# Kernel tuning notes

Measured on AMD Instinct MI355X. Metric: run time of the kernel, lower is better.

The kernel has to match this reference:

```python
import jax, jax.numpy as jnp
import numpy as np

B, T, P, N, E = 8, 12, 1000, 20000, 60000
FP, FN, H = 32, 32, 12  # patch feats, node feats, horizon
IN_DIM = (FP + FN) * T
HID = IN_DIM


def setup_inputs() -> dict:
    key = jax.random.key(0)
    ks = jax.random.split(key, 8)
    patch_x = jax.random.normal(ks[0], (B, T, P, FP), dtype=jnp.float32)
    nodes_x = jax.random.normal(ks[1], (B, T, N, FN), dtype=jnp.float32)
    subgraphs_batch = jax.random.randint(ks[2], (E,), 0, P)
    subgraphs_nodes_mapper = jax.random.randint(ks[3], (E,), 0, N)
    # 2-layer MLP: Linear(IN_DIM->HID) + ReLU + Linear(HID->H), no final activation
    s1 = 1.0 / np.sqrt(IN_DIM)
    s2 = 1.0 / np.sqrt(HID)
    W1 = jax.random.uniform(ks[4], (IN_DIM, HID), minval=-s1, maxval=s1, dtype=jnp.float32)
    b1 = jax.random.uniform(ks[5], (HID,), minval=-s1, maxval=s1, dtype=jnp.float32)
    W2 = jax.random.uniform(ks[6], (HID, H), minval=-s2, maxval=s2, dtype=jnp.float32)
    b2 = jax.random.uniform(ks[7], (H,), minval=-s2, maxval=s2, dtype=jnp.float32)
    return {"patch_x": patch_x, "nodes_x": nodes_x,
            "subgraphs_batch": subgraphs_batch,
            "subgraphs_nodes_mapper": subgraphs_nodes_mapper,
            "W1": W1, "b1": b1, "W2": W2, "b2": b2}


def reference(patch_x, nodes_x, subgraphs_batch, subgraphs_nodes_mapper, W1, b1, W2, b2):
    # gather patch features per membership entry: (B,T,E,FP)
    gathered = patch_x[:, :, subgraphs_batch, :]
    # scatter-mean over entries into nodes (segment reduction on entry axis)
    g = jnp.transpose(gathered, (2, 0, 1, 3))  # (E,B,T,FP)
    sums = jax.ops.segment_sum(g, subgraphs_nodes_mapper, num_segments=N)  # (N,B,T,FP)
    counts = jax.ops.segment_sum(jnp.ones((E,), jnp.float32), subgraphs_nodes_mapper, num_segments=N)
    mean = sums / jnp.maximum(counts, 1.0)[:, None, None, None]
    patch_x_nodes = jnp.transpose(mean, (1, 2, 0, 3))  # (B,T,N,FP)
    # rearrange 'B t n f -> B n (t f)'
    pxn = jnp.transpose(patch_x_nodes, (0, 2, 1, 3)).reshape(B, N, T * FP)
    nx = jnp.transpose(nodes_x, (0, 2, 1, 3)).reshape(B, N, T * FN)
    mlp_in = jnp.concatenate([nx, pxn], axis=-1)  # (B,N,IN_DIM)
    h = jax.nn.relu(jnp.einsum('bnd,dh->bnh', mlp_in, W1) + b1)
    out = jnp.einsum('bnh,ho->bno', h, W2) + b2  # (B,N,H)
    return out
```

## Files before the change

kernel.cpp:

```cpp
#include <hip/hip_runtime.h>

#define B_ 8
#define T_ 12
#define P_ 1000
#define N_ 20000
#define E_ 60000
#define FP_ 32
#define FN_ 32
#define HO_ 12
#define IND 768
#define M_ (B_*N_)

typedef __attribute__((ext_vector_type(8))) short bf16x8;
typedef __attribute__((ext_vector_type(4))) float f32x4;

__device__ __forceinline__ unsigned short f2bf(float x) {
    union { float f; unsigned int u; } v; v.f = x;
    unsigned int u = v.u;
    u += 0x7fffu + ((u >> 16) & 1u);
    return (unsigned short)(u >> 16);
}

#define GLDS16(gp, lp) \
    __builtin_amdgcn_global_load_lds((const __attribute__((address_space(1))) void*)(gp), \
                                     (__attribute__((address_space(3))) void*)(lp), 16, 0, 0)

__global__ void k_count(const int* __restrict__ mapper, int* __restrict__ counts) {
    int e = blockIdx.x * 256 + threadIdx.x;
    if (e < E_) atomicAdd(&counts[mapper[e]], 1);
}

__global__ __launch_bounds__(1024) void k_scan(const int* __restrict__ counts,
                                               int* __restrict__ offsets,
                                               int* __restrict__ cursor) {
    __shared__ int ps[1024];
    const int tid = threadIdx.x;
    const int CH = 20;
    const int base = tid * CH;
    int s = 0;
    for (int i = 0; i < CH; ++i) { int idx = base + i; if (idx < N_) s += counts[idx]; }
    ps[tid] = s;
    __syncthreads();
    for (int off = 1; off < 1024; off <<= 1) {
        int v = ps[tid];
        int a = (tid >= off) ? ps[tid - off] : 0;
        __syncthreads();
        ps[tid] = v + a;
        __syncthreads();
    }
    int run = (tid > 0) ? ps[tid - 1] : 0;
    for (int i = 0; i < CH; ++i) {
        int idx = base + i;
        if (idx < N_) { offsets[idx] = run; cursor[idx] = run; run += counts[idx]; }
    }
    if (tid == 1023) offsets[N_] = ps[1023];
}

__global__ void k_scatter(const int* __restrict__ mapper, const int* __restrict__ batch,
                          int* __restrict__ cursor, int* __restrict__ edge_p) {
    int e = blockIdx.x * 256 + threadIdx.x;
    if (e < E_) {
        int pos = atomicAdd(&cursor[mapper[e]], 1);
        edge_p[pos] = batch[e];
    }
}

__global__ void k_wprep(const float* __restrict__ W1, const float* __restrict__ W2,
                        unsigned short* __restrict__ W1t, unsigned short* __restrict__ W2t) {
    int i = blockIdx.x * 256 + threadIdx.x;
    if (i < IND * IND) {
        int h = i / IND, d = i - h * IND;
        W1t[i] = f2bf(W1[d * IND + h]);
    } else {
        int j = i - IND * IND;
        if (j < 16 * IND) {
            int o = j / IND, k = j - o * IND;
            W2t[j] = (o < HO_) ? f2bf(W2[k * HO_ + o]) : (unsigned short)0;
        }
    }
}

__global__ __launch_bounds__(256) void k_stage(const float* __restrict__ patch_x,
                                               const float* __restrict__ nodes_x,
                                               const int* __restrict__ offsets,
                                               const int* __restrict__ edge_p,
                                               unsigned short* __restrict__ X) {
    const int gw = (blockIdx.x * 256 + threadIdx.x) >> 6;
    const int lane = threadIdx.x & 63;
    const int b = gw / N_;
    const int n = gw - b * N_;
    unsigned short* xr = X + (size_t)gw * IND;

    int tt[3], ff[3];
    #pragma unroll
    for (int j = 0; j < 3; ++j) {
        const int c = 2 * (j * 64 + lane);
        tt[j] = c >> 5; ff[j] = c & 31;
    }

    const float* nb = nodes_x + ((size_t)b * T_ * N_ + n) * FN_;
    #pragma unroll
    for (int j = 0; j < 3; ++j) {
        float2 v = *(const float2*)(nb + (size_t)tt[j] * (N_ * FN_) + ff[j]);
        unsigned int pk = (unsigned int)f2bf(v.x) | ((unsigned int)f2bf(v.y) << 16);
        *(unsigned int*)(xr + 2 * (j * 64 + lane)) = pk;
    }

    const int s = offsets[n];
    const int cnt = offsets[n + 1] - s;
    int p_l = 0;
    if (lane < cnt) p_l = edge_p[s + lane];
    float2 acc[3] = {{0.f,0.f},{0.f,0.f},{0.f,0.f}};
    const float* pb0 = patch_x + (size_t)b * (T_ * P_ * FP_);
    const int m = cnt < 64 ? cnt : 64;
    for (int q = 0; q < m; ++q) {
        const int p = __shfl(p_l, q);
        const float* pe = pb0 + p * FP_;
        #pragma unroll
        for (int j = 0; j < 3; ++j) {
            float2 v = *(const float2*)(pe + (size_t)tt[j] * (P_ * FP_) + ff[j]);
            acc[j].x += v.x; acc[j].y += v.y;
        }
    }
    for (int q = 64; q < cnt; ++q) {
        const int p = edge_p[s + q];
        const float* pe = pb0 + p * FP_;
        #pragma unroll
        for (int j = 0; j < 3; ++j) {
            float2 v = *(const float2*)(pe + (size_t)tt[j] * (P_ * FP_) + ff[j]);
            acc[j].x += v.x; acc[j].y += v.y;
        }
    }
    const float inv = cnt > 0 ? 1.0f / (float)cnt : 0.0f;
    #pragma unroll
    for (int j = 0; j < 3; ++j) {
        unsigned int pk = (unsigned int)f2bf(acc[j].x * inv) |
                          ((unsigned int)f2bf(acc[j].y * inv) << 16);
        *(unsigned int*)(xr + 384 + 2 * (j * 64 + lane)) = pk;
    }
}

__global__ __launch_bounds__(256, 2) void k_gemm1(const unsigned short* __restrict__ X,
                                                  const unsigned short* __restrict__ W1t,
                                                  const float* __restrict__ b1,
                                                  const unsigned short* __restrict__ W2t,
                                                  float* __restrict__ part) {
    __shared__ __align__(16) unsigned short smem[16384];
    unsigned short* As = smem;
    unsigned short* Bs = smem + 8192;
    unsigned short* Hs = smem;

    const int id = blockIdx.x;
    const int q8 = 7500 >> 3, r8 = 7500 & 7;
    const int xcd = id & 7, pos = id >> 3;
    const int nid = (xcd < r8) ? xcd * (q8 + 1) + pos
                               : r8 * (q8 + 1) + (xcd - r8) * q8 + pos;
    const int colt = nid % 6;
    const int rowt = nid / 6;
    const int col0 = colt * 128;
    const int row0 = rowt * 128;

    const int t = threadIdx.x;
    const int lane = t & 63;
    const int w = t >> 6;
    const int wr = w >> 1, wc = w & 1;
    const int l15 = lane & 15;
    const int lhi = lane >> 4;

    f32x4 acc[4][4] = {};

    for (int kt = 0; kt < 12; ++kt) {
        const int k0 = kt * 64;
        #pragma unroll
        for (int i = 0; i < 4; ++i) {
            const int f = i * 2048 + t * 8;
            GLDS16(X + (row0 + (f >> 6)) * IND + k0 + (f & 63), &As[f]);
        }
        #pragma unroll
        for (int i = 0; i < 4; ++i) {
            const int f = i * 2048 + t * 8;
            GLDS16(W1t + (col0 + (f >> 6)) * IND + k0 + (f & 63), &Bs[f]);
        }
        __syncthreads();
        #pragma unroll
        for (int kk = 0; kk < 2; ++kk) {
            const int ko = kk * 32 + lhi * 8;
            bf16x8 af[4], bfr[4];
            #pragma unroll
            for (int m = 0; m < 4; ++m)
                af[m] = *(const bf16x8*)&As[(wr * 64 + m * 16 + l15) * 64 + ko];
            #pragma unroll
            for (int n = 0; n < 4; ++n)
                bfr[n] = *(const bf16x8*)&Bs[(wc * 64 + n * 16 + l15) * 64 + ko];
            #pragma unroll
            for (int m = 0; m < 4; ++m)
                #pragma unroll
                for (int n = 0; n < 4; ++n)
                    acc[m][n] = __builtin_amdgcn_mfma_f32_16x16x32_bf16(af[m], bfr[n], acc[m][n], 0, 0, 0);
        }
        __syncthreads();
    }

    #pragma unroll
    for (int n = 0; n < 4; ++n) {
        const int lcol = wc * 64 + n * 16 + l15;
        const float bb = b1[col0 + lcol];
        #pragma unroll
        for (int m = 0; m < 4; ++m) {
            #pragma unroll
            for (int r = 0; r < 4; ++r) {
                const int lrow = wr * 64 + m * 16 + lhi * 4 + r;
                float v = acc[m][n][r] + bb;
                v = v > 0.f ? v : 0.f;
                Hs[lrow * 128 + lcol] = f2bf(v);
            }
        }
    }
    __syncthreads();

    f32x4 p0 = {}, p1 = {};
    #pragma unroll
    for (int kk = 0; kk < 4; ++kk) {
        const int ko = kk * 32 + lhi * 8;
        bf16x8 bw = *(const bf16x8*)&W2t[l15 * IND + col0 + ko];
        bf16x8 a0 = *(const bf16x8*)&Hs[(w * 32 + l15) * 128 + ko];
        bf16x8 a1 = *(const bf16x8*)&Hs[(w * 32 + 16 + l15) * 128 + ko];
        p0 = __builtin_amdgcn_mfma_f32_16x16x32_bf16(a0, bw, p0, 0, 0, 0);
        p1 = __builtin_amdgcn_mfma_f32_16x16x32_bf16(a1, bw, p1, 0, 0, 0);
    }
    if (l15 < HO_) {
        float* pp = part + (size_t)colt * ((size_t)M_ * HO_);
        #pragma unroll
        for (int r = 0; r < 4; ++r) {
            const int g0 = row0 + w * 32 + lhi * 4 + r;
            pp[(size_t)g0 * HO_ + l15] = p0[r];
            pp[(size_t)(g0 + 16) * HO_ + l15] = p1[r];
        }
    }
}

__global__ void k_reduce(const float* __restrict__ part, const float* __restrict__ b2,
                         float* __restrict__ out) {
    int i = blockIdx.x * 256 + threadIdx.x;
    if (i < M_ * HO_) {
        const int o = i % HO_;
        float s = b2[o];
        #pragma unroll
        for (int ct = 0; ct < 6; ++ct) s += part[(size_t)ct * ((size_t)M_ * HO_) + i];
        out[i] = s;
    }
}

extern "C" void kernel_launch(void* const* d_in, const int* in_sizes, int n_in,
                              void* d_out, int out_size, void* d_ws, size_t ws_size,
                              hipStream_t stream) {
    const float* patch_x = (const float*)d_in[0];
    const float* nodes_x = (const float*)d_in[1];
    const int*   sb      = (const int*)d_in[2];
    const int*   snm     = (const int*)d_in[3];
    const float* W1      = (const float*)d_in[4];
    const float* b1      = (const float*)d_in[5];
    const float* W2      = (const float*)d_in[6];
    const float* b2      = (const float*)d_in[7];
    float* out = (float*)d_out;

    char* ws = (char*)d_ws;
    size_t off = 0;
    auto alloc = [&](size_t bytes) -> void* {
        void* p = ws + off;
        off = (off + bytes + 255) & ~(size_t)255;
        return p;
    };
    int* counts  = (int*)alloc((size_t)N_ * 4);
    int* offsets = (int*)alloc((size_t)(N_ + 1) * 4);
    int* cursor  = (int*)alloc((size_t)N_ * 4);
    int* edge_p  = (int*)alloc((size_t)E_ * 4);
    unsigned short* W1t = (unsigned short*)alloc((size_t)IND * IND * 2);
    unsigned short* W2t = (unsigned short*)alloc((size_t)16 * IND * 2);
    unsigned short* X   = (unsigned short*)alloc((size_t)M_ * IND * 2);
    float* part         = (float*)alloc((size_t)6 * M_ * HO_ * 4);

    hipMemsetAsync(counts, 0, (size_t)N_ * 4, stream);
    k_count  <<<(E_ + 255) / 256, 256, 0, stream>>>(snm, counts);
    k_scan   <<<1, 1024, 0, stream>>>(counts, offsets, cursor);
    k_scatter<<<(E_ + 255) / 256, 256, 0, stream>>>(snm, sb, cursor, edge_p);
    k_wprep  <<<(IND * IND + 16 * IND) / 256, 256, 0, stream>>>(W1, W2, W1t, W2t);
    k_stage  <<<M_ / 4, 256, 0, stream>>>(patch_x, nodes_x, offsets, edge_p, X);
    k_gemm1  <<<7500, 256, 0, stream>>>(X, W1t, b1, W2t, part);
    k_reduce <<<(M_ * HO_ + 255) / 256, 256, 0, stream>>>(part, b2, out);
}
```

Measured before the change: 722.6 us.

## Rewrite GEMM1 as 256x256-tile double-buffered pipelined kernel with swizzled LDS

The fused GEMM1+GEMM2 kernel moves from 128x128 tiles with 256 threads to 256x256 tiles with 512 threads (8 waves). It double-buffers global-to-LDS loads across K steps, interleaving them with MFMA quarters under explicit barriers, waitcnts and setprio. LDS is XOR-swizzled to avoid bank conflicts. Wider column tiles halve the partial-sum buffer and the reduce passes (6 to 3). The cost is one block per CU with 128KB LDS, higher register pressure, and a hand-scheduled sync pattern that is fragile.

After: 690.2 us. -4.5%, faster.

```diff
diff --git a/kernel.cpp b/kernel.cpp
--- a/kernel.cpp
+++ b/kernel.cpp
@@ -140,91 +140,148 @@
     }
 }
 
-__global__ __launch_bounds__(256, 2) void k_gemm1(const unsigned short* __restrict__ X,
+
+#define BARRIER() __builtin_amdgcn_s_barrier()
+#define LGKM0()  { asm volatile("s_waitcnt lgkmcnt(0)" ::: "memory"); __builtin_amdgcn_sched_barrier(0); }
+#define VMC(n)   { asm volatile("s_waitcnt vmcnt(" #n ")" ::: "memory"); }
+
+__global__ __launch_bounds__(512, 1) void k_gemm1(const unsigned short* __restrict__ X,
                                                   const unsigned short* __restrict__ W1t,
                                                   const float* __restrict__ b1,
                                                   const unsigned short* __restrict__ W2t,
                                                   float* __restrict__ part) {
-    __shared__ __align__(16) unsigned short smem[16384];
-    unsigned short* As = smem;
-    unsigned short* Bs = smem + 8192;
-    unsigned short* Hs = smem;
+    __shared__ __align__(16) unsigned short lds[65536];
 
     const int id = blockIdx.x;
-    const int q8 = 7500 >> 3, r8 = 7500 & 7;
     const int xcd = id & 7, pos = id >> 3;
-    const int nid = (xcd < r8) ? xcd * (q8 + 1) + pos
-                               : r8 * (q8 + 1) + (xcd - r8) * q8 + pos;
-    const int colt = nid % 6;
-    const int rowt = nid / 6;
-    const int col0 = colt * 128;
-    const int row0 = rowt * 128;
+    const int nid = (xcd < 3) ? xcd * 235 + pos : 3 * 235 + (xcd - 3) * 234 + pos;
+    const int colt = nid % 3;
+    const int rowt = nid / 3;
+    const int row0 = rowt * 256;
+    const int col0 = colt * 256;
 
     const int t = threadIdx.x;
     const int lane = t & 63;
     const int w = t >> 6;
-    const int wr = w >> 1, wc = w & 1;
+    const int wm = w >> 2;
+    const int wn = w & 3;
     const int l15 = lane & 15;
     const int lhi = lane >> 4;
 
-    f32x4 acc[4][4] = {};
-
-    for (int kt = 0; kt < 12; ++kt) {
-        const int k0 = kt * 64;
-        #pragma unroll
-        for (int i = 0; i < 4; ++i) {
-            const int f = i * 2048 + t * 8;
-            GLDS16(X + (row0 + (f >> 6)) * IND + k0 + (f & 63), &As[f]);
-        }
-        #pragma unroll
-        for (int i = 0; i < 4; ++i) {
-            const int f = i * 2048 + t * 8;
-            GLDS16(W1t + (col0 + (f >> 6)) * IND + k0 + (f & 63), &Bs[f]);
-        }
-        __syncthreads();
-        #pragma unroll
-        for (int kk = 0; kk < 2; ++kk) {
-            const int ko = kk * 32 + lhi * 8;
-            bf16x8 af[4], bfr[4];
-            #pragma unroll
-            for (int m = 0; m < 4; ++m)
-                af[m] = *(const bf16x8*)&As[(wr * 64 + m * 16 + l15) * 64 + ko];
-            #pragma unroll
-            for (int n = 0; n < 4; ++n)
-                bfr[n] = *(const bf16x8*)&Bs[(wc * 64 + n * 16 + l15) * 64 + ko];
-            #pragma unroll
-            for (int m = 0; m < 4; ++m)
-                #pragma unroll
-                for (int n = 0; n < 4; ++n)
-                    acc[m][n] = __builtin_amdgcn_mfma_f32_16x16x32_bf16(af[m], bfr[n], acc[m][n], 0, 0, 0);
-        }
-        __syncthreads();
+    const int sr = t >> 3;
+    const int sc = (t & 7) ^ (sr & 7);
+    const int arow = wm * 128 + l15;
+    const int brow = wn * 64 + l15;
+    const int axor = l15 & 7;
+
+#define STAGE(k, sec, hf) { \
+        const unsigned short* _s = (sec) ? (W1t + (size_t)(col0 + (hf)*128 + sr) * IND + (k)*64 + sc*8) \
+                                         : (X   + (size_t)(row0 + (hf)*128 + sr) * IND + (k)*64 + sc*8); \
+        unsigned short* _d = &lds[(((k)&1) << 15) + ((sec) << 14) + ((hf) << 13) + t*8]; \
+        GLDS16(_s, _d); \
+        GLDS16(_s + (size_t)64*IND, _d + 4096); }
+
+#define LDA4(buf, mlo) \
+        _Pragma("unroll") for (int m_ = 0; m_ < 4; ++m_) \
+        _Pragma("unroll") for (int ks_ = 0; ks_ < 2; ++ks_) \
+            a_reg[(mlo)+m_][ks_] = *(const bf16x8*)&lds[((buf) << 15) + (arow + ((mlo)+m_)*16)*64 + (((ks_*4+lhi) ^ axor) << 3)];
+
+#define LDB2(buf, nlo) \
+        _Pragma("unroll") for (int n_ = 0; n_ < 2; ++n_) \
+        _Pragma("unroll") for (int ks_ = 0; ks_ < 2; ++ks_) \
+            b_reg[(nlo)+n_][ks_] = *(const bf16x8*)&lds[((buf) << 15) + 16384 + (brow + ((nlo)+n_)*16)*64 + (((ks_*4+lhi) ^ axor) << 3)];
+
+#define MFMA_Q(mlo, nlo) \
+        __builtin_amdgcn_s_setprio(1); \
+        _Pragma("unroll") for (int m_ = 0; m_ < 4; ++m_) \
+        _Pragma("unroll") for (int n_ = 0; n_ < 2; ++n_) \
+        _Pragma("unroll") for (int ks_ = 0; ks_ < 2; ++ks_) \
+            acc[(mlo)+m_][(nlo)+n_] = __builtin_amdgcn_mfma_f32_16x16x32_bf16( \
+                a_reg[(mlo)+m_][ks_], b_reg[(nlo)+n_][ks_], acc[(mlo)+m_][(nlo)+n_], 0, 0, 0); \
+        __builtin_amdgcn_s_setprio(0);
+
+    f32x4 acc[8][4] = {};
+    bf16x8 a_reg[8][2], b_reg[4][2];
+
+    STAGE(0, 0, 0); STAGE(0, 0, 1); STAGE(0, 1, 0); STAGE(0, 1, 1);
+    STAGE(1, 0, 0); STAGE(1, 0, 1);
+    VMC(4);
+    BARRIER();
+
+    for (int it = 0; it < 6; ++it) {
+        const int a = 2 * it, b = 2 * it + 1;
+        const bool more = (it < 5);
+        LDA4(0, 0); LDB2(0, 0);
+        STAGE(b, 1, 0);
+        BARRIER(); LGKM0();
+        MFMA_Q(0, 0);
+        BARRIER();
+        LDA4(0, 4);
+        STAGE(b, 1, 1);
+        BARRIER(); LGKM0();
+        MFMA_Q(4, 0);
+        BARRIER();
+        LDB2(0, 2);
+        if (more) STAGE(a + 2, 0, 0);
+        BARRIER(); LGKM0();
+        MFMA_Q(0, 2);
+        BARRIER();
+        if (more) STAGE(a + 2, 0, 1);
+        BARRIER();
+        MFMA_Q(4, 2);
+        if (more) { VMC(4); } else { VMC(0); }
+        BARRIER();
+        LDA4(1, 0); LDB2(1, 0);
+        if (more) STAGE(a + 2, 1, 0);
+        BARRIER(); LGKM0();
+        MFMA_Q(0, 0);
+        BARRIER();
+        LDA4(1, 4);
+        if (more) STAGE(a + 2, 1, 1);
+        BARRIER(); LGKM0();
+        MFMA_Q(4, 0);
+        BARRIER();
+        LDB2(1, 2);
+        if (more) STAGE(b + 2, 0, 0);
+        BARRIER(); LGKM0();
+        MFMA_Q(0, 2);
+        BARRIER();
+        if (more) STAGE(b + 2, 0, 1);
+        BARRIER();
+        MFMA_Q(4, 2);
+        if (more) { VMC(4); } else { VMC(0); }
+        BARRIER();
     }
 
     #pragma unroll
     for (int n = 0; n < 4; ++n) {
-        const int lcol = wc * 64 + n * 16 + l15;
-        const float bb = b1[col0 + lcol];
-        #pragma unroll
-        for (int m = 0; m < 4; ++m) {
+        const int col = wn * 64 + n * 16 + l15;
+        const float bb = b1[col0 + col];
+        const int c8 = col >> 3, c7 = col & 7;
+        #pragma unroll
+        for (int m = 0; m < 8; ++m) {
             #pragma unroll
             for (int r = 0; r < 4; ++r) {
-                const int lrow = wr * 64 + m * 16 + lhi * 4 + r;
+                const int row = wm * 128 + m * 16 + lhi * 4 + r;
                 float v = acc[m][n][r] + bb;
                 v = v > 0.f ? v : 0.f;
-                Hs[lrow * 128 + lcol] = f2bf(v);
+                lds[row * 256 + ((c8 ^ (row & 7)) << 3) + c7] = f2bf(v);
             }
         }
     }
-    __syncthreads();
+    asm volatile("s_waitcnt lgkmcnt(0)" ::: "memory");
+    BARRIER();
 
     f32x4 p0 = {}, p1 = {};
-    #pragma unroll
-    for (int kk = 0; kk < 4; ++kk) {
-        const int ko = kk * 32 + lhi * 8;
-        bf16x8 bw = *(const bf16x8*)&W2t[l15 * IND + col0 + ko];
-        bf16x8 a0 = *(const bf16x8*)&Hs[(w * 32 + l15) * 128 + ko];
-        bf16x8 a1 = *(const bf16x8*)&Hs[(w * 32 + 16 + l15) * 128 + ko];
+    const int er0 = w * 32 + l15;
+    const int er1 = er0 + 16;
+    const int ex = er0 & 7;
+    #pragma unroll
+    for (int kk = 0; kk < 8; ++kk) {
+        const int kc = kk * 4 + lhi;
+        bf16x8 bw = *(const bf16x8*)&W2t[l15 * IND + col0 + kk * 32 + lhi * 8];
+        bf16x8 a0 = *(const bf16x8*)&lds[er0 * 256 + ((kc ^ ex) << 3)];
+        bf16x8 a1 = *(const bf16x8*)&lds[er1 * 256 + ((kc ^ ex) << 3)];
         p0 = __builtin_amdgcn_mfma_f32_16x16x32_bf16(a0, bw, p0, 0, 0, 0);
         p1 = __builtin_amdgcn_mfma_f32_16x16x32_bf16(a1, bw, p1, 0, 0, 0);
     }
@@ -237,6 +294,10 @@
             pp[(size_t)(g0 + 16) * HO_ + l15] = p1[r];
         }
     }
+#undef STAGE
+#undef LDA4
+#undef LDB2
+#undef MFMA_Q
 }
 
 __global__ void k_reduce(const float* __restrict__ part, const float* __restrict__ b2,
@@ -246,7 +307,7 @@
         const int o = i % HO_;
         float s = b2[o];
         #pragma unroll
-        for (int ct = 0; ct < 6; ++ct) s += part[(size_t)ct * ((size_t)M_ * HO_) + i];
+        for (int ct = 0; ct < 3; ++ct) s += part[(size_t)ct * ((size_t)M_ * HO_) + i];
         out[i] = s;
     }
 }
@@ -278,7 +339,7 @@
     unsigned short* W1t = (unsigned short*)alloc((size_t)IND * IND * 2);
     unsigned short* W2t = (unsigned short*)alloc((size_t)16 * IND * 2);
     unsigned short* X   = (unsigned short*)alloc((size_t)M_ * IND * 2);
-    float* part         = (float*)alloc((size_t)6 * M_ * HO_ * 4);
+    float* part         = (float*)alloc((size_t)3 * M_ * HO_ * 4);
 
     hipMemsetAsync(counts, 0, (size_t)N_ * 4, stream);
     k_count  <<<(E_ + 255) / 256, 256, 0, stream>>>(snm, counts);
@@ -286,6 +347,6 @@
     k_scatter<<<(E_ + 255) / 256, 256, 0, stream>>>(snm, sb, cursor, edge_p);
     k_wprep  <<<(IND * IND + 16 * IND) / 256, 256, 0, stream>>>(W1, W2, W1t, W2t);
     k_stage  <<<M_ / 4, 256, 0, stream>>>(patch_x, nodes_x, offsets, edge_p, X);
-    k_gemm1  <<<7500, 256, 0, stream>>>(X, W1t, b1, W2t, part);
+    k_gemm1  <<<1875, 512, 0, stream>>>(X, W1t, b1, W2t, part);
     k_reduce <<<(M_ * HO_ + 255) / 256, 256, 0, stream>>>(part, b2, out);
 }
```
